# Kernel tuning notes

Measured on AMD Instinct MI355X. Metric: run time of the kernel, lower is better.

Reference implementation:

```python
import jax, jax.numpy as jnp
import numpy as np

B, T, N, F, NH, K = 512, 32, 64, 32, 4, 4
D = N * F          # model_dim = 2048
GH = N             # GRU hidden = num_channels
EPS_BN = 1e-5
EPS_LN = 1e-5


def _normalize_A(A):
    # relu -> zero diag -> symmetrize -> sym-normalized Laplacian -> rescale (lmax=2)
    n = A.shape[-1]
    eye = jnp.eye(n, dtype=A.dtype)
    A = jax.nn.relu(A) * (1.0 - eye)
    A = A + A.T
    dinv = 1.0 / jnp.sqrt(jnp.sum(A, axis=1) + 1e-10)
    L = eye - dinv[:, None] * A * dinv[None, :]
    return 2.0 * L / 2.0 - eye


def _cheby(L, k):
    # Chebyshev polynomial basis T_0..T_{k-1} of L, stacked [k, N, N]
    n = L.shape[-1]
    sup = [jnp.eye(n, dtype=L.dtype), L]
    for _ in range(2, k):
        sup.append(2.0 * L @ sup[-1] - sup[-2])
    return jnp.stack(sup[:k])


def _bn(x, g, b, axes):
    # training-mode batch norm (biased variance), stats over `axes`
    m = jnp.mean(x, axes, keepdims=True)
    v = jnp.mean((x - m) ** 2, axes, keepdims=True)
    return (x - m) / jnp.sqrt(v + EPS_BN) * g + b


def _forward(x, A, cheb_W, bn1_g, bn1_b, bn2_g, bn2_b,
             Wq, Wk, Wv, Wf, bf, ln_g, ln_b,
             W_ih, W_hh, b_ih, b_hh, lin_W, lin_b, cls_W, cls_b):
    Bsz, Tn, Nn, Fn = x.shape
    xt = jnp.swapaxes(x, 0, 1)                                   # [T,B,N,F]
    # DGCNN BN1: stats over (B, N) per feature, per time step
    xb = _bn(xt, bn1_g[:, None, None, :], bn1_b[:, None, None, :], (1, 2))
    # per-timestep normalized Laplacian and Chebyshev basis
    Ls = jax.vmap(_normalize_A)(A)                               # [T,N,N]
    cheb = jax.vmap(lambda L: _cheby(L, K))(Ls)                  # [T,K,N,N]
    # Chebynet: sum_k (T_k(L) @ x) @ W_k, then relu
    res = jnp.einsum('tknm,tbmf,tkfo->tbno', cheb, xb, cheb_W)   # [T,B,N,F]
    res = jax.nn.relu(res)
    # per-timestep BatchNorm over flattened (B*N, F)
    y = res.reshape(Tn, Bsz * Nn, Fn)
    y = _bn(y, bn2_g[:, None, :], bn2_b[:, None, :], (1,))
    y = jax.nn.sigmoid(y)                                        # [T,B*N,F]
    # replicate torch's stack/transpose/reshape exactly
    y_seq = jnp.swapaxes(y, 0, 1).reshape(Bsz, Tn, Nn * Fn)      # [B,T,D]
    # multi-head attention (no bias on q/k/v, scale = dh^-0.5)
    dh = D // NH
    def heads(z, W):
        return jnp.swapaxes((z @ W).reshape(Bsz, Tn, NH, dh), 1, 2)  # [B,H,T,dh]
    q, k, v = heads(y_seq, Wq), heads(y_seq, Wk), heads(y_seq, Wv)
    attn = jax.nn.softmax(jnp.einsum('bhqd,bhkd->bhqk', q, k) * dh ** -0.5, axis=-1)
    ctx = jnp.einsum('bhqk,bhkd->bhqd', attn, v)
    ctx = jnp.swapaxes(ctx, 1, 2).reshape(Bsz, Tn, D)
    out = ctx @ Wf + bf
    h = y_seq + out
    mu = jnp.mean(h, -1, keepdims=True)
    var = jnp.mean((h - mu) ** 2, -1, keepdims=True)
    h = (h - mu) / jnp.sqrt(var + EPS_LN) * ln_g + ln_b          # [B,T,D]
    # GRU (torch gate convention), scan over time
    def step(hprev, xt_):
        gi = xt_ @ W_ih.T + b_ih                                  # [B,3H]
        gh = hprev @ W_hh.T + b_hh
        ir, iz, inn = jnp.split(gi, 3, axis=-1)
        hr, hz, hn = jnp.split(gh, 3, axis=-1)
        r = jax.nn.sigmoid(ir + hr)
        zg = jax.nn.sigmoid(iz + hz)
        ng = jnp.tanh(inn + r * hn)
        hnew = (1.0 - zg) * ng + zg * hprev
        return hnew, hnew
    h0 = jnp.zeros((Bsz, GH), x.dtype)
    _, hs = jax.lax.scan(step, h0, jnp.swapaxes(h, 0, 1))        # [T,B,GH]
    y_gru = jax.nn.sigmoid(jnp.swapaxes(hs, 0, 1))               # [B,T,GH]
    out_flat = y_gru.reshape(Bsz, Tn * GH)
    proj = jax.nn.sigmoid(out_flat @ lin_W.T + lin_b)
    proj = proj / jnp.maximum(jnp.linalg.norm(proj, axis=-1, keepdims=True), 1e-12)
    y_pred = jax.nn.sigmoid(out_flat @ cls_W.T + cls_b)
    return proj[:, None, :], y_pred


def setup_inputs() -> dict:
    key = jax.random.key(0)
    ks = jax.random.split(key, 12)
    def nrm(k, shape, s):
        return jax.random.normal(k, shape, dtype=jnp.float32) * s
    return {
        'x': jax.random.normal(ks[0], (B, T, N, F), dtype=jnp.float32),
        'A': jax.random.uniform(ks[1], (T, N, N), minval=0.01, maxval=0.5, dtype=jnp.float32),
        'cheb_W': nrm(ks[2], (T, K, F, F), 0.1),
        'bn1_g': jnp.ones((T, F), jnp.float32), 'bn1_b': jnp.zeros((T, F), jnp.float32),
        'bn2_g': jnp.ones((T, F), jnp.float32), 'bn2_b': jnp.zeros((T, F), jnp.float32),
        'Wq': nrm(ks[3], (D, D), 0.02), 'Wk': nrm(ks[4], (D, D), 0.02), 'Wv': nrm(ks[5], (D, D), 0.02),
        'Wf': nrm(ks[6], (D, D), 0.02), 'bf': jnp.zeros((D,), jnp.float32),
        'ln_g': jnp.ones((D,), jnp.float32), 'ln_b': jnp.zeros((D,), jnp.float32),
        'W_ih': nrm(ks[7], (3 * GH, D), 0.02), 'W_hh': nrm(ks[8], (3 * GH, GH), 0.1),
        'b_ih': jnp.zeros((3 * GH,), jnp.float32), 'b_hh': jnp.zeros((3 * GH,), jnp.float32),
        'lin_W': nrm(ks[9], (128, T * GH), 0.05), 'lin_b': jnp.zeros((128,), jnp.float32),
        'cls_W': nrm(ks[10], (3, T * GH), 0.05), 'cls_b': jnp.zeros((3,), jnp.float32),
    }


def reference(x, A, cheb_W, bn1_g, bn1_b, bn2_g, bn2_b,
              Wq, Wk, Wv, Wf, bf, ln_g, ln_b,
              W_ih, W_hh, b_ih, b_hh, lin_W, lin_b, cls_W, cls_b):
    return _forward(x, A, cheb_W, bn1_g, bn1_b, bn2_g, bn2_b,
                    Wq, Wk, Wv, Wf, bf, ln_g, ln_b,
                    W_ih, W_hh, b_ih, b_hh, lin_W, lin_b, cls_W, cls_b)
```

## Files before the change

### kernel.cpp

```cpp
#include <hip/hip_runtime.h>
#include <hip/hip_bf16.h>

typedef unsigned short u16;
typedef __attribute__((ext_vector_type(8))) short short8;
typedef __attribute__((ext_vector_type(4))) short short4_;
typedef __attribute__((ext_vector_type(4))) float f32x4;

__device__ __forceinline__ u16 f2bf(float f){
  union { float fv; unsigned int u; } v; v.fv = f;
  unsigned int u = v.u;
  u = u + 0x7FFFu + ((u >> 16) & 1u);
  return (u16)(u >> 16);
}
__device__ __forceinline__ float bf2f(u16 h){
  union { unsigned int u; float fv; } v; v.u = ((unsigned int)h) << 16; return v.fv;
}
__device__ __forceinline__ float sigmoidf_(float x){ return 1.f/(1.f + __expf(-x)); }
__device__ __forceinline__ float tanhf_(float x){ return 2.f/(1.f + __expf(-2.f*x)) - 1.f; }

__device__ __forceinline__ void gload16(const void* g, void* l){
  __builtin_amdgcn_global_load_lds(
      (const __attribute__((address_space(1))) void*)g,
      (__attribute__((address_space(3))) void*)l, 16, 0, 0);
}
__device__ __forceinline__ f32x4 mfma_bf16(short8 a, short8 b, f32x4 c){
  return __builtin_amdgcn_mfma_f32_16x16x32_bf16(a, b, c, 0, 0, 0);
}

#define ASM_VMCNT8 asm volatile("s_waitcnt vmcnt(8)" ::: "memory")
#define ASM_VMCNT0 asm volatile("s_waitcnt vmcnt(0)" ::: "memory")
#define ASM_LGK0   asm volatile("s_waitcnt lgkmcnt(0)" ::: "memory")
#define SCHB       __builtin_amdgcn_sched_barrier(0)
#define SBAR       do { asm volatile("" ::: "memory"); __builtin_amdgcn_s_barrier(); asm volatile("" ::: "memory"); } while(0)

constexpr size_t OFF_A    = 0;
constexpr size_t OFF_B    = 67108864;
constexpr size_t OFF_C    = OFF_B + 67108864;
constexpr size_t OFF_D    = OFF_C + 201326592;
constexpr size_t OFF_E    = OFF_D + 67108864;
constexpr size_t OFF_WFT  = OFF_E + 25165824;
constexpr size_t OFF_WIH  = OFF_WFT + 8388608;
constexpr size_t OFF_LHAT = OFF_WIH + 1048576;
constexpr size_t OFF_B1P  = OFF_LHAT + 524288;
constexpr size_t OFF_B1S  = OFF_B1P + 524288;
constexpr size_t OFF_B2P  = OFF_B1S + 8192;
constexpr size_t OFF_B2S  = OFF_B2P + 4194304;
constexpr size_t OFF_TC   = OFF_LHAT;
constexpr size_t OFF_WT2  = OFF_C;
constexpr size_t OFF_GI   = OFF_C;
constexpr size_t OFF_OUTF = OFF_C + 16777216;

__global__ __launch_bounds__(256) void wtrans_kernel(const float* __restrict__ Wq, const float* __restrict__ Wk,
                                                     const float* __restrict__ Wv, const float* __restrict__ Wf,
                                                     u16* __restrict__ WqkvT, u16* __restrict__ WfT)
{
  const int k0 = blockIdx.x*64, n0 = blockIdx.y*64, z = blockIdx.z;
  const float* src = (z==0)?Wq:(z==1)?Wk:(z==2)?Wv:Wf;
  u16* dst = (z<3) ? (WqkvT + (size_t)z*2048*2048) : WfT;
  __shared__ float tile[64][65];
  const int c = threadIdx.x & 63, r0 = threadIdx.x >> 6;
#pragma unroll
  for (int i=0;i<16;++i){ int r = r0 + i*4; tile[r][c] = src[(size_t)(k0+r)*2048 + n0 + c]; }
  __syncthreads();
#pragma unroll
  for (int i=0;i<16;++i){ int r = r0 + i*4; dst[(size_t)(n0+r)*2048 + k0 + c] = f2bf(tile[c][r]); }
}

__global__ __launch_bounds__(256) void wih_kernel(const float* __restrict__ Wih, u16* __restrict__ WT)
{
  const int row = blockIdx.x, tid = threadIdx.x;
#pragma unroll
  for (int i=0;i<8;++i){ int col = tid + i*256;
    float v = (row < 192) ? Wih[(size_t)row*2048 + col] : 0.f;
    WT[(size_t)row*2048 + col] = f2bf(v);
  }
}

__global__ __launch_bounds__(256) void bn1_part_kernel(const float* __restrict__ x, float* __restrict__ part)
{
  const int t = blockIdx.x, sl = blockIdx.y;
  const int f = threadIdx.x & 31, grp = threadIdx.x >> 5;
  float s = 0.f, ss = 0.f;
  for (int bb = 0; bb < 8; ++bb){
    const int b = sl*8 + bb;
    const float* xp = x + ((size_t)(b*32 + t))*2048;
    for (int i = 0; i < 8; ++i){
      int n = i*8 + grp;
      float v = xp[n*32 + f];
      s += v; ss += v*v;
    }
  }
  __shared__ float red[8][32][2];
  red[grp][f][0] = s; red[grp][f][1] = ss;
  __syncthreads();
  if (threadIdx.x < 32){
    float S=0, SS=0;
    for (int g=0; g<8; ++g){ S += red[g][threadIdx.x][0]; SS += red[g][threadIdx.x][1]; }
    size_t o = (((size_t)t*64 + sl)*32 + threadIdx.x)*2;
    part[o] = S; part[o+1] = SS;
  }
}

__global__ __launch_bounds__(256) void bn1_fin_kernel(const float* __restrict__ part, const float* __restrict__ g1,
                                                      const float* __restrict__ b1, float* __restrict__ out)
{
  const int t = blockIdx.x;
  const int f = threadIdx.x & 31, grp = threadIdx.x >> 5;
  float s=0, ss=0;
  for (int sl = grp; sl < 64; sl += 8){
    size_t o = (((size_t)t*64 + sl)*32 + f)*2;
    s += part[o]; ss += part[o+1];
  }
  __shared__ float red[8][32][2];
  red[grp][f][0]=s; red[grp][f][1]=ss;
  __syncthreads();
  if (threadIdx.x < 32){
    float S=0, SS=0;
    for (int g=0; g<8; ++g){ S+=red[g][threadIdx.x][0]; SS+=red[g][threadIdx.x][1]; }
    float mean = S*(1.f/32768.f);
    float var  = SS*(1.f/32768.f) - mean*mean;
    float sc   = g1[t*32+threadIdx.x]*rsqrtf(var + 1e-5f);
    out[(t*32+threadIdx.x)*2]   = sc;
    out[(t*32+threadIdx.x)*2+1] = b1[t*32+threadIdx.x] - mean*sc;
  }
}

__global__ __launch_bounds__(256) void lap2_kernel(const float* __restrict__ A, const float* __restrict__ chebW,
                                                   u16* __restrict__ Tcat, u16* __restrict__ WTg)
{
  const int t = blockIdx.x, tid = threadIdx.x;
  __shared__ float Ar[64][68];
  __shared__ float L1[64][68];
  __shared__ float T2s[64][68];
  __shared__ float dr[64];
#pragma unroll
  for (int i=0;i<16;++i){ int idx = tid + i*256; int r = idx>>6, c = idx&63;
    float v = A[(size_t)t*4096 + idx]; v = fmaxf(v, 0.f); if (r==c) v = 0.f;
    Ar[r][c] = v; }
  __syncthreads();
  if (tid < 64){
    float s = 0;
    for (int c2=0;c2<64;++c2) s += Ar[tid][c2] + Ar[c2][tid];
    dr[tid] = rsqrtf(s + 1e-10f);
  }
  __syncthreads();
#pragma unroll
  for (int i=0;i<16;++i){ int idx = tid + i*256; int r = idx>>6, c = idx&63;
    L1[r][c] = -(Ar[r][c] + Ar[c][r]) * dr[r] * dr[c];
  }
  __syncthreads();
  const int row = tid >> 2, c0 = (tid & 3) << 4;
  float a2[16];
#pragma unroll
  for (int j=0;j<16;++j) a2[j] = 0.f;
#pragma unroll 4
  for (int m=0;m<64;++m){
    float lv = L1[row][m];
#pragma unroll
    for (int j=0;j<16;++j) a2[j] += lv*L1[m][c0+j];
  }
#pragma unroll
  for (int j=0;j<16;++j) T2s[row][c0+j] = 2.f*a2[j] - ((row==c0+j)?1.f:0.f);
  __syncthreads();
  float a3[16];
#pragma unroll
  for (int j=0;j<16;++j) a3[j] = 0.f;
#pragma unroll 4
  for (int m=0;m<64;++m){
    float lv = L1[row][m];
#pragma unroll
    for (int j=0;j<16;++j) a3[j] += lv*T2s[m][c0+j];
  }
  u16* tb = Tcat + (size_t)t*16384 + row*256;
#pragma unroll
  for (int j=0;j<16;++j){
    int c = c0 + j;
    tb[c]       = f2bf((row==c)?1.f:0.f);
    tb[64 + c]  = f2bf(L1[row][c]);
    tb[128 + c] = f2bf(T2s[row][c]);
    tb[192 + c] = f2bf(2.f*a3[j] - L1[row][c]);
  }
#pragma unroll
  for (int i=0;i<16;++i){
    int idx = tid + i*256;
    int k = idx>>10, f = (idx>>5)&31, fo = idx&31;
    WTg[(size_t)t*4096 + k*1024 + fo*32 + f] = f2bf(chebW[(size_t)t*4096 + idx]);
  }
}

__global__ __launch_bounds__(256) void cheby_kernel(const float* __restrict__ x, const u16* __restrict__ Tcat,
                                                    const u16* __restrict__ WTg, const float* __restrict__ bn1ss,
                                                    u16* __restrict__ Rb, float* __restrict__ bn2p)
{
  const int t = blockIdx.x >> 6, grp = blockIdx.x & 63, b0 = grp*8;
  const int tid = threadIdx.x, wid = tid >> 6, lane = tid & 63;
  const int fr = lane & 15, fk = (lane >> 4) << 3;
  const int cc = lane & 15, cr = (lane >> 4) << 2;

  __shared__ u16 Tc[64][264];
  __shared__ u16 Wt[128][40];
  __shared__ u16 Xs[64][40];
  __shared__ u16 Gt[128][72];
  __shared__ float red[4][32][2];
  __shared__ float scs[64];

  if (tid < 64) scs[tid] = bn1ss[t*64 + tid];
  {
    const u16* src = Tcat + (size_t)t*16384;
#pragma unroll
    for (int i=0;i<8;++i){ int idx = tid + i*256; int r = idx>>5, c8 = (idx&31)<<3;
      *(short8*)&Tc[r][c8] = *(const short8*)&src[r*256 + c8]; }
  }
  {
    const u16* src = WTg + (size_t)t*4096;
#pragma unroll
    for (int i=0;i<2;++i){ int idx = tid + i*256; int r = idx>>2, c8 = (idx&3)<<3;
      *(short8*)&Wt[r][c8] = *(const short8*)&src[r*32 + c8]; }
  }
  __syncthreads();

  for (int bb=0; bb<8; ++bb){
    const int b = b0 + bb;
    {
      const float* xr = x + ((size_t)(b*32 + t))*2048;
      f32x4 v0 = *(const f32x4*)&xr[tid*8];
      f32x4 v1 = *(const f32x4*)&xr[tid*8+4];
      const int fb = (tid*8)&31;
      short8 w;
#pragma unroll
      for (int e=0;e<4;++e){
        w[e]   = (short)f2bf(v0[e]*scs[2*(fb+e)]   + scs[2*(fb+e)+1]);
        w[e+4] = (short)f2bf(v1[e]*scs[2*(fb+4+e)] + scs[2*(fb+4+e)+1]);
      }
      *(short8*)&Xs[tid>>2][(tid&3)<<3] = w;
    }
    __syncthreads();
    {
      f32x4 g[4][2] = {};
      short8 xa[4], wb[2];
#pragma unroll
      for (int m2=0;m2<4;++m2) xa[m2] = *(const short8*)&Xs[m2*16 + fr][fk];
#pragma unroll
      for (int j=0;j<2;++j)    wb[j]  = *(const short8*)&Wt[wid*32 + j*16 + fr][fk];
#pragma unroll
      for (int m2=0;m2<4;++m2)
#pragma unroll
        for (int j=0;j<2;++j) g[m2][j] = mfma_bf16(xa[m2], wb[j], g[m2][j]);
#pragma unroll
      for (int m2=0;m2<4;++m2)
#pragma unroll
        for (int j=0;j<2;++j){
          short4_ q;
#pragma unroll
          for (int r=0;r<4;++r) q[r] = (short)f2bf(g[m2][j][r]);
          *(short4_*)&Gt[wid*32 + j*16 + cc][m2*16 + cr] = q;
        }
    }
    __syncthreads();
    f32x4 racc[2] = {};
#pragma unroll
    for (int ks=0; ks<8; ++ks){
      short8 ta  = *(const short8*)&Tc[wid*16 + fr][ks*32 + fk];
      short8 gb0 = *(const short8*)&Gt[(ks>>1)*32 + fr][(ks&1)*32 + fk];
      short8 gb1 = *(const short8*)&Gt[(ks>>1)*32 + 16 + fr][(ks&1)*32 + fk];
      racc[0] = mfma_bf16(ta, gb0, racc[0]);
      racc[1] = mfma_bf16(ta, gb1, racc[1]);
    }
    u16* rrow = Rb + ((size_t)(t*512 + b))*2048;
    float sev[2], sqv[2];
#pragma unroll
    for (int j=0;j<2;++j){
      float s1=0.f, s2=0.f;
#pragma unroll
      for (int r=0;r<4;++r){
        float v = fmaxf(racc[j][r], 0.f);
        rrow[(wid*16 + cr + r)*32 + j*16 + cc] = f2bf(v);
        s1 += v; s2 += v*v;
      }
      sev[j]=s1; sqv[j]=s2;
    }
#pragma unroll
    for (int j=0;j<2;++j){
      sev[j] += __shfl_xor(sev[j], 16, 64); sev[j] += __shfl_xor(sev[j], 32, 64);
      sqv[j] += __shfl_xor(sqv[j], 16, 64); sqv[j] += __shfl_xor(sqv[j], 32, 64);
    }
    if (lane < 16){
#pragma unroll
      for (int j=0;j<2;++j){ red[wid][j*16+cc][0] = sev[j]; red[wid][j*16+cc][1] = sqv[j]; }
    }
    __syncthreads();
    if (tid < 64){
      int f = tid & 31, c = tid >> 5;
      bn2p[((size_t)(t*512+b)*32 + f)*2 + c] = red[0][f][c]+red[1][f][c]+red[2][f][c]+red[3][f][c];
    }
    __syncthreads();
  }
}

__global__ __launch_bounds__(256) void bn2_fin_kernel(const float* __restrict__ part, const float* __restrict__ g2,
                                                      const float* __restrict__ b2, float* __restrict__ out)
{
  const int t = blockIdx.x;
  const int f = threadIdx.x & 31, grp = threadIdx.x >> 5;
  float s=0, ss=0;
  for (int b = grp; b < 512; b += 8){
    size_t o = ((size_t)(t*512+b)*32 + f)*2;
    s += part[o]; ss += part[o+1];
  }
  __shared__ float red[8][32][2];
  red[grp][f][0]=s; red[grp][f][1]=ss;
  __syncthreads();
  if (threadIdx.x < 32){
    float S=0, SS=0;
    for (int g=0; g<8; ++g){ S+=red[g][threadIdx.x][0]; SS+=red[g][threadIdx.x][1]; }
    float mean = S*(1.f/32768.f);
    float var  = SS*(1.f/32768.f) - mean*mean;
    float scv  = g2[t*32+threadIdx.x]*rsqrtf(var + 1e-5f);
    out[(t*32+threadIdx.x)*2]   = scv;
    out[(t*32+threadIdx.x)*2+1] = b2[t*32+threadIdx.x] - mean*scv;
  }
}

__global__ __launch_bounds__(256) void bn2apply_kernel(const u16* __restrict__ Rb, const float* __restrict__ ss,
                                                       u16* __restrict__ YS)
{
  const int t = blockIdx.x >> 9, b = blockIdx.x & 511, tid = threadIdx.x;
  __shared__ float scs[64];
  if (tid < 64) scs[tid] = ss[t*64 + tid];
  __syncthreads();
  const int n = tid >> 2, f0 = (tid & 3) << 3;
  short8 rv = *(const short8*)&Rb[((size_t)(t*512+b))*2048 + tid*8];
  short8 w;
#pragma unroll
  for (int e=0;e<8;++e){
    int f = f0 + e;
    float v = bf2f((u16)rv[e])*scs[f*2] + scs[f*2+1];
    w[e] = (short)f2bf(sigmoidf_(v));
  }
  *(short8*)&YS[((size_t)(b*32 + (n>>1)))*2048 + (n&1)*1024 + t*32 + f0] = w;
}

template<int CB>
__global__ __launch_bounds__(512, 2) void gemm256_kernel(const u16* __restrict__ A, const u16* __restrict__ BT,
                                                         void* __restrict__ C, int M, int N, int K)
{
  __shared__ u16 smem[65536];
  const int tid = threadIdx.x, wid = tid >> 6, lane = tid & 63;
  const int MB = M >> 8, NB = N >> 8;
  const int xcd = (int)blockIdx.x & 7, q = (int)blockIdx.x >> 3;
  const int ppx = NB >> 3;
  const int mb = q / ppx, nb = xcd*ppx + q % ppx;
  (void)MB;
  const int m0 = mb << 8, n0g = nb << 8;
  const int nkt = K >> 6;
  const int nit = nkt >> 1;

  const int wr = wid >> 2, wc = wid & 3;
  const int fr = lane & 15, fk = (lane >> 4) << 3;
  const int cz0 = fk ^ ((fr & 7) << 3);
  const int cz1 = (32 + fk) ^ ((fr & 7) << 3);
  const int srow = wid*16 + (lane >> 3);
  const int scol = ((lane & 7) ^ (lane >> 3)) << 3;
  const int bhalf = wc >> 1, brow0 = (wc & 1) << 6;

  f32x4 acc[8][4] = {};
  short8 af[4][2], bg[4][2];

#define STG(PTR, R0, DSTB, TK, H) do { if ((TK) < nkt) { \
  const u16* _g = (PTR) + (size_t)((R0) + ((H)<<7) + srow)*(size_t)K + (size_t)(((TK)<<6) + scol); \
  u16* _d = &smem[(DSTB) + ((H)<<13) + (wid<<10)]; \
  gload16(_g, _d); gload16(_g + ((size_t)K<<3), _d + 512); } } while(0)

#define DSA(BUF, QM) { _Pragma("unroll") for(int m2=0;m2<4;++m2){ \
  const u16* _p = &smem[(BUF) + wr*8192 + (((QM)*64 + m2*16 + fr)<<6)]; \
  af[m2][0] = *(const short8*)(_p + cz0); af[m2][1] = *(const short8*)(_p + cz1); } }

#define DSB(BUF, QN) { _Pragma("unroll") for(int n2=0;n2<2;++n2){ \
  const u16* _p = &smem[(BUF) + 16384 + bhalf*8192 + ((brow0 + (QN)*32 + n2*16 + fr)<<6)]; \
  bg[(QN)*2+n2][0] = *(const short8*)(_p + cz0); bg[(QN)*2+n2][1] = *(const short8*)(_p + cz1); } }

#define MMA(QM, QN) { __builtin_amdgcn_s_setprio(1); \
  _Pragma("unroll") for(int m2=0;m2<4;++m2) _Pragma("unroll") for(int n2=0;n2<2;++n2) { \
    acc[(QM)*4+m2][(QN)*2+n2] = mfma_bf16(af[m2][0], bg[(QN)*2+n2][0], acc[(QM)*4+m2][(QN)*2+n2]); \
    acc[(QM)*4+m2][(QN)*2+n2] = mfma_bf16(af[m2][1], bg[(QN)*2+n2][1], acc[(QM)*4+m2][(QN)*2+n2]); } \
  __builtin_amdgcn_s_setprio(0); }

  STG(BT, n0g, 16384, 0, 0); STG(BT, n0g, 16384, 0, 1);
  STG(A,  m0,  0,     0, 0); STG(A,  m0,  0,     0, 1);
  STG(BT, n0g, 49152, 1, 0); STG(BT, n0g, 49152, 1, 1);
  STG(A,  m0,  32768, 1, 0); STG(A,  m0,  32768, 1, 1);
  ASM_VMCNT8; SBAR;

  for (int i = 0; i < nit; ++i){
    const int kb = i*2;
    DSA(0, 0); DSB(0, 0);
    SBAR; ASM_LGK0; SCHB; MMA(0,0); SBAR;
    DSB(0, 1);
    SBAR; ASM_LGK0; SCHB; MMA(0,1); SBAR;
    DSA(0, 1);
    STG(BT, n0g, 16384, kb+2, 0); STG(BT, n0g, 16384, kb+2, 1);
    SBAR; ASM_LGK0; SCHB; MMA(1,0); SBAR;
    STG(A, m0, 0, kb+2, 0); STG(A, m0, 0, kb+2, 1);
    if (kb + 2 >= nkt) { ASM_VMCNT0; } else { ASM_VMCNT8; }
    SBAR; MMA(1,1); SBAR;
    DSA(32768, 0); DSB(32768, 0);
    SBAR; ASM_LGK0; SCHB; MMA(0,0); SBAR;
    DSB(32768, 1);
    SBAR; ASM_LGK0; SCHB; MMA(0,1); SBAR;
    DSA(32768, 1);
    STG(BT, n0g, 49152, kb+3, 0); STG(BT, n0g, 49152, kb+3, 1);
    SBAR; ASM_LGK0; SCHB; MMA(1,0); SBAR;
    STG(A, m0, 32768, kb+3, 0); STG(A, m0, 32768, kb+3, 1);
    if (kb + 3 >= nkt) { ASM_VMCNT0; } else { ASM_VMCNT8; }
    SBAR; MMA(1,1); SBAR;
  }

#undef STG
#undef DSA
#undef DSB
#undef MMA

  const int cr = (lane >> 4) << 2, cc = lane & 15;
#pragma unroll
  for (int mf=0; mf<8; ++mf)
#pragma unroll
    for (int nf=0; nf<4; ++nf)
#pragma unroll
      for (int r=0; r<4; ++r){
        const size_t row = (size_t)(m0 + wr*128 + mf*16 + cr + r);
        const size_t col = (size_t)(n0g + wc*64 + nf*16 + cc);
        if (CB == 0) ((u16*)C)[row*(size_t)N + col] = f2bf(acc[mf][nf][r]);
        else        ((float*)C)[row*(size_t)N + col] = acc[mf][nf][r];
      }
}

template<int CB>
__global__ __launch_bounds__(256) void gemm_bt_kernel(const u16* __restrict__ A, const u16* __restrict__ BT,
                                                      void* __restrict__ C, int M, int N, int K)
{
  __shared__ u16 As[128*32];
  __shared__ u16 Bs[128*32];
  const int tid = threadIdx.x;
  const int wave = tid >> 6, lane = tid & 63;
  const int mblocks = M >> 7;
  const int mb = blockIdx.x % mblocks;
  const int nb = blockIdx.x / mblocks;
  const int lr = lane >> 2;
  const int lc = (lane & 3) << 3;
  const u16* Ag0 = A  + (size_t)(mb*128 + wave*16 + lr)*K + lc;
  const u16* Bg0 = BT + (size_t)(nb*128 + wave*16 + lr)*K + lc;
  const u16* Ag1 = Ag0 + (size_t)64*K;
  const u16* Bg1 = Bg0 + (size_t)64*K;
  u16* lA0 = &As[(wave*16)*32];
  u16* lA1 = &As[(wave*16+64)*32];
  u16* lB0 = &Bs[(wave*16)*32];
  u16* lB1 = &Bs[(wave*16+64)*32];
  const int wm = (wave >> 1)*64, wn = (wave & 1)*64;
  const int fr = lane & 15, fk = (lane >> 4) << 3;
  f32x4 acc[4][4] = {};
  for (int kt = 0; kt < K; kt += 32){
    __syncthreads();
    gload16(Ag0 + kt, lA0);
    gload16(Ag1 + kt, lA1);
    gload16(Bg0 + kt, lB0);
    gload16(Bg1 + kt, lB1);
    __syncthreads();
    short8 af[4], bfr[4];
#pragma unroll
    for (int i=0;i<4;++i) af[i]  = *(const short8*)&As[(wm + i*16 + fr)*32 + fk];
#pragma unroll
    for (int j=0;j<4;++j) bfr[j] = *(const short8*)&Bs[(wn + j*16 + fr)*32 + fk];
#pragma unroll
    for (int i=0;i<4;++i)
#pragma unroll
      for (int j=0;j<4;++j)
        acc[i][j] = mfma_bf16(af[i], bfr[j], acc[i][j]);
  }
  const int cr = (lane >> 4) << 2, cc = lane & 15;
#pragma unroll
  for (int i=0;i<4;++i)
#pragma unroll
    for (int j=0;j<4;++j)
#pragma unroll
      for (int r=0;r<4;++r){
        const size_t row = (size_t)(mb*128 + wm + i*16 + cr + r);
        const size_t col = (size_t)(nb*128 + wn + j*16 + cc);
        if (CB == 0) ((u16*)C)[row*(size_t)N + col] = f2bf(acc[i][j][r]);
        else        ((float*)C)[row*(size_t)N + col] = acc[i][j][r];
      }
}

__global__ __launch_bounds__(256) void attn_kernel(const u16* __restrict__ QKV, u16* __restrict__ CTX)
{
  const int b = blockIdx.x >> 2, h = blockIdx.x & 3;
  const int tid = threadIdx.x;
  const int wave = tid >> 6, lane = tid & 63;
  __shared__ float spart[4][32][33];
  __shared__ float sm[32][33];
  __shared__ float rowinv[32];
  __shared__ u16 pb[32][40];
  __shared__ u16 vt[512][40];

  {
    const int t2 = tid >> 3;
    const size_t vbase = ((size_t)(b*32 + t2))*6144 + 4096 + h*512;
#pragma unroll
    for (int i = 0; i < 8; ++i){
      int d0 = i*64 + (tid & 7)*8;
      short8 v8 = *(const short8*)&QKV[vbase + d0];
#pragma unroll
      for (int e = 0; e < 8; ++e) vt[d0+e][t2] = (u16)v8[e];
    }
  }
  const int fr = lane & 15, fk = (lane >> 4) << 3;
  f32x4 sacc[2][2] = {};
  const size_t qrow = ((size_t)(b*32))*6144 + h*512;
#pragma unroll
  for (int kk = 0; kk < 4; ++kk){
    const int kof = wave*128 + kk*32 + fk;
    short8 qf0 = *(const short8*)&QKV[qrow + (size_t)fr*6144 + kof];
    short8 qf1 = *(const short8*)&QKV[qrow + (size_t)(fr+16)*6144 + kof];
    short8 kf0 = *(const short8*)&QKV[qrow + 2048 + (size_t)fr*6144 + kof];
    short8 kf1 = *(const short8*)&QKV[qrow + 2048 + (size_t)(fr+16)*6144 + kof];
    sacc[0][0] = mfma_bf16(qf0, kf0, sacc[0][0]);
    sacc[0][1] = mfma_bf16(qf0, kf1, sacc[0][1]);
    sacc[1][0] = mfma_bf16(qf1, kf0, sacc[1][0]);
    sacc[1][1] = mfma_bf16(qf1, kf1, sacc[1][1]);
  }
  const int cr = (lane >> 4) << 2, cc = lane & 15;
#pragma unroll
  for (int i=0;i<2;++i)
#pragma unroll
    for (int j=0;j<2;++j)
#pragma unroll
      for (int r=0;r<4;++r) spart[wave][i*16+cr+r][j*16+cc] = sacc[i][j][r];
  __syncthreads();
  const float scl = 0.04419417382415922f;
  for (int e = tid; e < 1024; e += 256){
    int r = e >> 5, c = e & 31;
    sm[r][c] = (spart[0][r][c]+spart[1][r][c]+spart[2][r][c]+spart[3][r][c])*scl;
  }
  __syncthreads();
  if (tid < 32){
    float m = -1e30f;
    for (int c=0;c<32;++c) m = fmaxf(m, sm[tid][c]);
    float s = 0;
    for (int c=0;c<32;++c){ float e = __expf(sm[tid][c]-m); sm[tid][c] = e; s += e; }
    rowinv[tid] = 1.f/s;
  }
  __syncthreads();
  for (int e = tid; e < 1024; e += 256){
    int r = e>>5, c = e&31;
    pb[r][c] = f2bf(sm[r][c]*rowinv[r]);
  }
  __syncthreads();
  f32x4 cacc[2][8] = {};
  short8 pf0 = *(const short8*)&pb[fr][fk];
  short8 pf1 = *(const short8*)&pb[fr+16][fk];
#pragma unroll
  for (int j=0;j<8;++j){
    short8 vf = *(const short8*)&vt[wave*128 + j*16 + fr][fk];
    cacc[0][j] = mfma_bf16(pf0, vf, cacc[0][j]);
    cacc[1][j] = mfma_bf16(pf1, vf, cacc[1][j]);
  }
#pragma unroll
  for (int i=0;i<2;++i)
#pragma unroll
    for (int j=0;j<8;++j)
#pragma unroll
      for (int r=0;r<4;++r){
        int t1 = i*16 + cr + r;
        int d  = wave*128 + j*16 + cc;
        CTX[((size_t)(b*32+t1))*2048 + h*512 + d] = f2bf(cacc[i][j][r]);
      }
}

__global__ __launch_bounds__(256) void ln_kernel(const u16* __restrict__ OUT, const u16* __restrict__ YS,
                                                 const float* __restrict__ bfv, const float* __restrict__ lng,
                                                 const float* __restrict__ lnb, u16* __restrict__ HLN)
{
  const int row = blockIdx.x, tid = threadIdx.x;
  const size_t base = (size_t)row*2048 + tid*8;
  short8 o8 = *(const short8*)&OUT[base];
  short8 y8 = *(const short8*)&YS[base];
  float hv[8]; float s = 0;
#pragma unroll
  for (int e=0;e<8;++e){ float v = bf2f((u16)o8[e]) + bf2f((u16)y8[e]) + bfv[tid*8+e]; hv[e]=v; s += v; }
  __shared__ float red[4];
#pragma unroll
  for (int off=32; off; off>>=1) s += __shfl_down(s, off, 64);
  if ((tid&63)==0) red[tid>>6] = s;
  __syncthreads();
  const float mu = (red[0]+red[1]+red[2]+red[3]) * (1.f/2048.f);
  float s2 = 0;
#pragma unroll
  for (int e=0;e<8;++e){ float d = hv[e]-mu; s2 += d*d; }
  __syncthreads();
#pragma unroll
  for (int off=32; off; off>>=1) s2 += __shfl_down(s2, off, 64);
  if ((tid&63)==0) red[tid>>6] = s2;
  __syncthreads();
  const float rstd = rsqrtf((red[0]+red[1]+red[2]+red[3])*(1.f/2048.f) + 1e-5f);
  short8 w;
#pragma unroll
  for (int e=0;e<8;++e) w[e] = (short)f2bf((hv[e]-mu)*rstd*lng[tid*8+e] + lnb[tid*8+e]);
  *(short8*)&HLN[base] = w;
}

__global__ __launch_bounds__(256) void gru_kernel(const float* __restrict__ GI, const float* __restrict__ Whh,
                                                  const float* __restrict__ bih, const float* __restrict__ bhh,
                                                  float* __restrict__ OUTF)
{
  const int b = blockIdx.x, tid = threadIdx.x;
  __shared__ float w[192*65];
  __shared__ float hprev[64];
  __shared__ float gh[192];
#pragma unroll
  for (int i=0;i<48;++i){ int idx = tid + i*256; w[(idx>>6)*65 + (idx&63)] = Whh[idx]; }
  if (tid < 64) hprev[tid] = 0.f;
  const float bh_ = (tid<192) ? bhh[tid] : 0.f;
  __syncthreads();
  for (int t=0;t<32;++t){
    if (tid < 192){
      float s = bh_;
      const float* wr = &w[tid*65];
#pragma unroll 8
      for (int g=0; g<64; ++g) s += wr[g]*hprev[g];
      gh[tid] = s;
    }
    __syncthreads();
    if (tid < 64){
      const float* gi = GI + ((size_t)(b*32 + t))*256;
      float r  = sigmoidf_(gi[tid]     + bih[tid]     + gh[tid]);
      float z  = sigmoidf_(gi[tid+64]  + bih[tid+64]  + gh[tid+64]);
      float n  = tanhf_(gi[tid+128] + bih[tid+128] + r*gh[tid+128]);
      float hn = (1.f - z)*n + z*hprev[tid];
      hprev[tid] = hn;
      OUTF[(size_t)b*2048 + t*64 + tid] = sigmoidf_(hn);
    }
    __syncthreads();
  }
}

__global__ __launch_bounds__(256) void head_kernel(const float* __restrict__ OUTF, const float* __restrict__ linW,
                                                   const float* __restrict__ linb, const float* __restrict__ clsW,
                                                   const float* __restrict__ clsb, float* __restrict__ outp)
{
  const int b = blockIdx.x, tid = threadIdx.x;
  __shared__ float row[2048];
  __shared__ float pr[128];
  __shared__ float part[256];
  __shared__ float rn;
#pragma unroll
  for (int i=0;i<8;++i) row[tid + i*256] = OUTF[(size_t)b*2048 + tid + i*256];
  __syncthreads();
  {
    const int j = tid & 127, half = tid >> 7;
    const float* wr = linW + (size_t)j*2048 + half*1024;
    const float* xr = &row[half*1024];
    float s = 0;
    for (int k=0;k<1024;++k) s += xr[k]*wr[k];
    part[tid] = s;
  }
  __syncthreads();
  if (tid < 128){
    float v = part[tid] + part[tid+128] + linb[tid];
    v = sigmoidf_(v);
    pr[tid] = v;
    part[tid] = v*v;
  }
  __syncthreads();
  if (tid == 0){
    float ss = 0;
    for (int i2=0;i2<128;++i2) ss += part[i2];
    rn = 1.f/fmaxf(sqrtf(ss), 1e-12f);
  }
  __syncthreads();
  if (tid < 128) outp[(size_t)b*128 + tid] = pr[tid]*rn;
  if (tid < 192){
    const int c = tid >> 6, l = tid & 63;
    const float* wr = clsW + (size_t)c*2048;
    float s = 0;
    for (int k=l; k<2048; k+=64) s += row[k]*wr[k];
#pragma unroll
    for (int off=32; off; off>>=1) s += __shfl_down(s, off, 64);
    if (l == 0) outp[65536 + (size_t)b*3 + c] = sigmoidf_(s + clsb[c]);
  }
}

extern "C" void kernel_launch(void* const* d_in, const int* in_sizes, int n_in,
                              void* d_out, int out_size, void* d_ws, size_t ws_size,
                              hipStream_t stream) {
  const float* x    = (const float*)d_in[0];
  const float* Aadj = (const float*)d_in[1];
  const float* chbW = (const float*)d_in[2];
  const float* bn1g = (const float*)d_in[3];
  const float* bn1b = (const float*)d_in[4];
  const float* bn2g = (const float*)d_in[5];
  const float* bn2b = (const float*)d_in[6];
  const float* Wq   = (const float*)d_in[7];
  const float* Wk   = (const float*)d_in[8];
  const float* Wv   = (const float*)d_in[9];
  const float* Wf   = (const float*)d_in[10];
  const float* bfv  = (const float*)d_in[11];
  const float* lng  = (const float*)d_in[12];
  const float* lnb  = (const float*)d_in[13];
  const float* Wih  = (const float*)d_in[14];
  const float* Whh  = (const float*)d_in[15];
  const float* bih  = (const float*)d_in[16];
  const float* bhh  = (const float*)d_in[17];
  const float* linW = (const float*)d_in[18];
  const float* linb = (const float*)d_in[19];
  const float* clsW = (const float*)d_in[20];
  const float* clsb = (const float*)d_in[21];

  char* ws = (char*)d_ws;
  u16*   Rb    = (u16*)(ws + OFF_A);
  u16*   OUTB  = (u16*)(ws + OFF_A);
  u16*   YSEQ  = (u16*)(ws + OFF_B);
  u16*   QKV   = (u16*)(ws + OFF_C);
  u16*   CTX   = (u16*)(ws + OFF_D);
  u16*   HLN   = (u16*)(ws + OFF_D);
  u16*   WqkvT = (u16*)(ws + OFF_E);
  u16*   WfT   = (u16*)(ws + OFF_WFT);
  u16*   WihT  = (u16*)(ws + OFF_WIH);
  u16*   Tcat  = (u16*)(ws + OFF_TC);
  u16*   WTg   = (u16*)(ws + OFF_WT2);
  float* b1p   = (float*)(ws + OFF_B1P);
  float* b1s   = (float*)(ws + OFF_B1S);
  float* b2p   = (float*)(ws + OFF_B2P);
  float* b2s   = (float*)(ws + OFF_B2S);
  float* GI    = (float*)(ws + OFF_GI);
  float* OUTF  = (float*)(ws + OFF_OUTF);

  wtrans_kernel<<<dim3(32,32,4), 256, 0, stream>>>(Wq, Wk, Wv, Wf, WqkvT, WfT);
  wih_kernel<<<dim3(256), 256, 0, stream>>>(Wih, WihT);
  bn1_part_kernel<<<dim3(32,64), 256, 0, stream>>>(x, b1p);
  bn1_fin_kernel<<<dim3(32), 256, 0, stream>>>(b1p, bn1g, bn1b, b1s);
  lap2_kernel<<<dim3(32), 256, 0, stream>>>(Aadj, chbW, Tcat, WTg);
  cheby_kernel<<<dim3(2048), 256, 0, stream>>>(x, Tcat, WTg, b1s, Rb, b2p);
  bn2_fin_kernel<<<dim3(32), 256, 0, stream>>>(b2p, bn2g, bn2b, b2s);
  bn2apply_kernel<<<dim3(16384), 256, 0, stream>>>(Rb, b2s, YSEQ);
  gemm256_kernel<0><<<dim3(1536), 512, 0, stream>>>(YSEQ, WqkvT, (void*)QKV, 16384, 6144, 2048);
  attn_kernel<<<dim3(2048), 256, 0, stream>>>(QKV, CTX);
  gemm256_kernel<0><<<dim3(512), 512, 0, stream>>>(CTX, WfT, (void*)OUTB, 16384, 2048, 2048);
  ln_kernel<<<dim3(16384), 256, 0, stream>>>(OUTB, YSEQ, bfv, lng, lnb, HLN);
  gemm_bt_kernel<1><<<dim3(256), 256, 0, stream>>>(HLN, WihT, (void*)GI, 16384, 256, 2048);
  gru_kernel<<<dim3(512), 256, 0, stream>>>(GI, Whh, bih, bhh, OUTF);
  head_kernel<<<dim3(512), 256, 0, stream>>>(OUTF, linW, linb, clsW, clsb, (float*)d_out);
}
```

Before: 955.9 us.

## Restructure GEMM k-tile loop to cut barriers and overlap LDS reads with MFMA

Rewrites the double-buffered GEMM main loop so each k-tile issues its LDS fragment reads up front, waits only partially (lgkmcnt(4)) before the first MFMA group, and runs MFMA groups back-to-back. It drops the per-MFMA-group barriers, keeping two barriers per tile around the global-to-LDS prefetch. The prefetch of the next tile into the same buffer is moved to after all reads of that buffer are done. The goal is to remove barrier stalls and hide LDS latency behind MFMA, at the cost of less interleaving between global prefetch and compute.

Result: no change. 971.2 us (+1.6%).

```diff
diff --git a/kernel.cpp b/kernel.cpp
--- a/kernel.cpp
+++ b/kernel.cpp
@@ -30,6 +30,7 @@
 #define ASM_VMCNT8 asm volatile("s_waitcnt vmcnt(8)" ::: "memory")
 #define ASM_VMCNT0 asm volatile("s_waitcnt vmcnt(0)" ::: "memory")
 #define ASM_LGK0   asm volatile("s_waitcnt lgkmcnt(0)" ::: "memory")
+#define ASM_LGK4   asm volatile("s_waitcnt lgkmcnt(4)" ::: "memory")
 #define SCHB       __builtin_amdgcn_sched_barrier(0)
 #define SBAR       do { asm volatile("" ::: "memory"); __builtin_amdgcn_s_barrier(); asm volatile("" ::: "memory"); } while(0)
 
@@ -385,6 +386,19 @@
     acc[(QM)*4+m2][(QN)*2+n2] = mfma_bf16(af[m2][1], bg[(QN)*2+n2][1], acc[(QM)*4+m2][(QN)*2+n2]); } \
   __builtin_amdgcn_s_setprio(0); }
 
+#define KTILE(BUF, TKNXT, DSTB) do { \
+  DSA(BUF, 0); DSB(BUF, 0); DSB(BUF, 1); \
+  ASM_LGK4; SCHB; MMA(0,0); \
+  ASM_LGK0; SCHB; MMA(0,1); \
+  DSA(BUF, 1); \
+  ASM_LGK0; SCHB; MMA(1,0); MMA(1,1); \
+  SBAR; \
+  STG(BT, n0g, (DSTB)+16384, (TKNXT), 0); STG(BT, n0g, (DSTB)+16384, (TKNXT), 1); \
+  STG(A,  m0,  (DSTB),        (TKNXT), 0); STG(A,  m0,  (DSTB),        (TKNXT), 1); \
+  if ((TKNXT) >= nkt) { ASM_VMCNT0; } else { ASM_VMCNT8; } \
+  SBAR; \
+} while(0)
+
   STG(BT, n0g, 16384, 0, 0); STG(BT, n0g, 16384, 0, 1);
   STG(A,  m0,  0,     0, 0); STG(A,  m0,  0,     0, 1);
   STG(BT, n0g, 49152, 1, 0); STG(BT, n0g, 49152, 1, 1);
@@ -393,28 +407,11 @@
 
   for (int i = 0; i < nit; ++i){
     const int kb = i*2;
-    DSA(0, 0); DSB(0, 0);
-    SBAR; ASM_LGK0; SCHB; MMA(0,0); SBAR;
-    DSB(0, 1);
-    SBAR; ASM_LGK0; SCHB; MMA(0,1); SBAR;
-    DSA(0, 1);
-    STG(BT, n0g, 16384, kb+2, 0); STG(BT, n0g, 16384, kb+2, 1);
-    SBAR; ASM_LGK0; SCHB; MMA(1,0); SBAR;
-    STG(A, m0, 0, kb+2, 0); STG(A, m0, 0, kb+2, 1);
-    if (kb + 2 >= nkt) { ASM_VMCNT0; } else { ASM_VMCNT8; }
-    SBAR; MMA(1,1); SBAR;
-    DSA(32768, 0); DSB(32768, 0);
-    SBAR; ASM_LGK0; SCHB; MMA(0,0); SBAR;
-    DSB(32768, 1);
-    SBAR; ASM_LGK0; SCHB; MMA(0,1); SBAR;
-    DSA(32768, 1);
-    STG(BT, n0g, 49152, kb+3, 0); STG(BT, n0g, 49152, kb+3, 1);
-    SBAR; ASM_LGK0; SCHB; MMA(1,0); SBAR;
-    STG(A, m0, 32768, kb+3, 0); STG(A, m0, 32768, kb+3, 1);
-    if (kb + 3 >= nkt) { ASM_VMCNT0; } else { ASM_VMCNT8; }
-    SBAR; MMA(1,1); SBAR;
-  }
-
+    KTILE(0,     kb+2, 0);
+    KTILE(32768, kb+3, 32768);
+  }
+
+#undef KTILE
 #undef STG
 #undef DSA
 #undef DSB
```
